# Kernel tuning notes

Hardware: AMD Instinct MI355X
Metric: run time of the kernel (lower is better)

Reference implementation:

```python
import jax, jax.numpy as jnp
import numpy as np

# Config constants (from DeepSeekConfig / init_kwargs)
NUM_EXPERTS = 6
VAR_EXPERTS = 4
FIXED_EXPERTS = NUM_EXPERTS - VAR_EXPERTS  # 2
TOP_K = 2
D_MODEL = 1024
D_FF = 4 * D_MODEL
LN_EPS = 1e-5


def setup_inputs() -> dict:
    key = jax.random.key(0)
    ks = jax.random.split(key, 6)
    B, S = 2, 2048
    x = jax.random.normal(ks[0], (B, S, D_MODEL), dtype=jnp.float32)
    router_W = jax.random.normal(ks[1], (D_MODEL, VAR_EXPERTS), dtype=jnp.float32) * 0.02
    # stacked expert FFN params: (E, D, 4D) and (E, 4D, D)
    W1 = jax.random.normal(ks[2], (NUM_EXPERTS, D_MODEL, D_FF), dtype=jnp.float32) * 0.02
    b1 = jnp.zeros((NUM_EXPERTS, D_FF), dtype=jnp.float32)
    W2 = jax.random.normal(ks[3], (NUM_EXPERTS, D_FF, D_MODEL), dtype=jnp.float32) * 0.02
    b2 = jnp.zeros((NUM_EXPERTS, D_MODEL), dtype=jnp.float32)
    ln_gamma = jnp.ones((D_MODEL,), dtype=jnp.float32)
    ln_beta = jnp.zeros((D_MODEL,), dtype=jnp.float32)
    return {"x": x, "router_W": router_W, "W1": W1, "b1": b1, "W2": W2,
            "b2": b2, "ln_gamma": ln_gamma, "ln_beta": ln_beta}


def reference(x, router_W, W1, b1, W2, b2, ln_gamma, ln_beta):
    B, S, D = x.shape
    # router over the VARIABLE experts only
    router_logits = jnp.einsum('bsd,de->bse', x, router_W)          # (B,S,VAR)
    router_probs = jax.nn.softmax(router_logits, axis=-1)
    _, topk_idx = jax.lax.top_k(router_probs, TOP_K)                 # (B,S,K)
    adj_idx = topk_idx + FIXED_EXPERTS                               # global expert ids in [FIXED, NUM)

    # dense per-expert FFN on all tokens: experts[e](x) = gelu(x@W1[e]+b1[e]) @ W2[e] + b2[e]
    h = jnp.einsum('bsd,edf->ebsf', x, W1) + b1[:, None, None, :]    # (E,B,S,4D)
    h = jax.nn.gelu(h, approximate=False)                            # torch F.gelu default = exact
    all_out = jnp.einsum('ebsf,efd->ebsd', h, W2) + b2[:, None, None, :]  # (E,B,S,D)

    # fixed experts: all of experts[0:FIXED] applied to every token
    fixed_sum = all_out[:FIXED_EXPERTS].sum(axis=0)                  # (B,S,D)

    # variable experts: per-token gather of the top-k selected experts
    b_ix = jnp.arange(B)[:, None, None]
    s_ix = jnp.arange(S)[None, :, None]
    var = all_out[adj_idx, b_ix, s_ix, :]                            # (B,S,K,D)

    # cat along expert slot dim then mean == sum / (FIXED + K); topk probs unused (plain mean)
    combined = (fixed_sum + var.sum(axis=2)) / (FIXED_EXPERTS + TOP_K)

    # LayerNorm (biased variance, eps=1e-5)
    mu = combined.mean(axis=-1, keepdims=True)
    v = combined.var(axis=-1, keepdims=True)
    out = (combined - mu) / jnp.sqrt(v + LN_EPS) * ln_gamma + ln_beta
    return out, router_logits
```

## Files before the change

### kernel.cpp

```cpp
#include <hip/hip_runtime.h>
#include <cstdint>
#include <cstddef>

#define D_MODEL 1024
#define D_FF 4096
#define NTOK 4096
#define LN_EPS 1e-5f

typedef __bf16 bf16x8 __attribute__((ext_vector_type(8)));
typedef float f32x4 __attribute__((ext_vector_type(4)));
typedef unsigned short u16x4 __attribute__((ext_vector_type(4)));
typedef unsigned short u16x8 __attribute__((ext_vector_type(8)));

static __device__ __forceinline__ unsigned short f2bf(float f) {
    union { float f; unsigned u; } v; v.f = f;
    unsigned r = v.u + 0x7fffu + ((v.u >> 16) & 1u);
    return (unsigned short)(r >> 16);
}

static __device__ __forceinline__ float b2f(unsigned short u) {
    union { unsigned u; float f; } v; v.u = (unsigned)u << 16;
    return v.f;
}

static __device__ __forceinline__ float gelu_fast(float x) {
    float x2 = x * x;
    float a2 = x * __builtin_fmaf(-0.1029432f, x2, -2.3022084f);
    float e = __builtin_amdgcn_exp2f(a2);
    return x * __builtin_amdgcn_rcpf(1.0f + e);
}

static __device__ __forceinline__ void gload16(const void* g, void* l) {
    __builtin_amdgcn_global_load_lds(
        (const __attribute__((address_space(1))) void*)g,
        (__attribute__((address_space(3))) void*)l, 16, 0, 0);
}

static __device__ __forceinline__ void seg_of(const int* cnt, int seg[4], int pc[4]) {
    int o = 2 * NTOK;
    #pragma unroll
    for (int e = 0; e < 4; ++e) {
        int c = cnt[e * 32];
        pc[e] = (c + 255) & ~255;
        seg[e] = o;
        o += pc[e];
    }
}

__global__ __launch_bounds__(256) void transpose_kernel(const float* __restrict__ W,
                                                        unsigned short* __restrict__ Wt,
                                                        int K, int N) {
    __shared__ unsigned short t[64][65];
    int k0 = blockIdx.y * 64, n0 = blockIdx.x * 64;
    const float* We = W + (size_t)blockIdx.z * K * N;
    unsigned short* Wte = Wt + (size_t)blockIdx.z * K * N;
    #pragma unroll
    for (int i = 0; i < 4; ++i) {
        int idx = threadIdx.x + i * 256;
        int kr = idx >> 4, c4 = idx & 15;
        f32x4 v = *(const f32x4*)&We[(size_t)(k0 + kr) * N + n0 + c4 * 4];
        #pragma unroll
        for (int j = 0; j < 4; ++j) t[c4 * 4 + j][kr] = f2bf(v[j]);
    }
    __syncthreads();
    #pragma unroll
    for (int i = 0; i < 2; ++i) {
        int idx = threadIdx.x + i * 256;
        int nr = idx >> 3, ck = idx & 7;
        u16x8 w;
        #pragma unroll
        for (int j = 0; j < 8; ++j) w[j] = t[nr][ck * 8 + j];
        *(u16x8*)&Wte[(size_t)(n0 + nr) * K + k0 + ck * 8] = w;
    }
}

__global__ __launch_bounds__(256) void router_kernel(
        const float* __restrict__ x, const float* __restrict__ rW,
        float* __restrict__ logits, int* __restrict__ selpk,
        int* __restrict__ slotpk, int* __restrict__ cnt, int* __restrict__ list,
        unsigned short* __restrict__ xb) {
    __shared__ int se[8];
    __shared__ int sslot[8];
    int wid = threadIdx.x >> 6, lane = threadIdx.x & 63;
    int t = blockIdx.x * 4 + wid;
    const float* xr = x + (size_t)t * D_MODEL;
    unsigned short* xbr = xb + (size_t)t * D_MODEL;
    float a0 = 0.f, a1 = 0.f, a2 = 0.f, a3 = 0.f;
    #pragma unroll
    for (int i = 0; i < 4; ++i) {
        int d4 = lane + i * 64;
        f32x4 xv = *(const f32x4*)&xr[d4 * 4];
        u16x4 bo;
        #pragma unroll
        for (int j = 0; j < 4; ++j) {
            float xj = xv[j];
            f32x4 wv = *(const f32x4*)&rW[(d4 * 4 + j) * 4];
            a0 = __builtin_fmaf(xj, wv[0], a0);
            a1 = __builtin_fmaf(xj, wv[1], a1);
            a2 = __builtin_fmaf(xj, wv[2], a2);
            a3 = __builtin_fmaf(xj, wv[3], a3);
            bo[j] = f2bf(xj);
        }
        *(u16x4*)&xbr[d4 * 4] = bo;
    }
    #pragma unroll
    for (int off = 32; off; off >>= 1) {
        a0 += __shfl_xor(a0, off); a1 += __shfl_xor(a1, off);
        a2 += __shfl_xor(a2, off); a3 += __shfl_xor(a3, off);
    }
    if (lane == 0) {
        float l[4] = {a0, a1, a2, a3};
        logits[t * 4 + 0] = a0; logits[t * 4 + 1] = a1;
        logits[t * 4 + 2] = a2; logits[t * 4 + 3] = a3;
        int e0 = 0; float b = l[0];
        #pragma unroll
        for (int e = 1; e < 4; ++e) if (l[e] > b) { b = l[e]; e0 = e; }
        int e1 = -1; float b2 = -1e30f;
        #pragma unroll
        for (int e = 0; e < 4; ++e) {
            if (e == e0) continue;
            if (l[e] > b2) { b2 = l[e]; e1 = e; }
        }
        se[wid * 2] = e0; se[wid * 2 + 1] = e1;
    }
    __syncthreads();
    if (threadIdx.x == 0) {
        int cnts[4] = {0, 0, 0, 0}, base[4];
        #pragma unroll
        for (int k = 0; k < 8; ++k) cnts[se[k]]++;
        #pragma unroll
        for (int e = 0; e < 4; ++e)
            if (cnts[e]) base[e] = atomicAdd(&cnt[e * 32], cnts[e]);
        int run[4] = {0, 0, 0, 0};
        #pragma unroll
        for (int k = 0; k < 8; ++k) {
            int e = se[k];
            int s = base[e] + run[e]++;
            sslot[k] = s;
            list[e * NTOK + s] = blockIdx.x * 4 + (k >> 1);
        }
    }
    __syncthreads();
    if (lane == 0) {
        selpk[t] = se[wid * 2] | (se[wid * 2 + 1] << 8);
        slotpk[t] = sslot[wid * 2] | (sslot[wid * 2 + 1] << 16);
    }
}

template<int GELU, int WM, int WN, int GX, int GY>
__global__ __launch_bounds__(512) void gemm_kernel(
        const unsigned short* __restrict__ A, const unsigned short* __restrict__ B,
        const float* __restrict__ bias, int bias_stride, int ldo,
        unsigned short* __restrict__ out,
        const int* __restrict__ cnt, const int* __restrict__ list, int K) {
    constexpr int BM = WM * 64, BN = WN * 64;
    __shared__ unsigned short As[BM * 64];
    __shared__ unsigned short Bs[BN * 64];

    const int D = blockIdx.x + GX * (blockIdx.y + GY * blockIdx.z);
    const int tq = D >> 3;
    const int W = ((D & 7) << 2) + ((tq >> 2) << 5) + (tq & 3);
    const int bx = W % GX;
    const int rem = W / GX;
    const int by = rem % GY;
    const int e  = rem / GY;

    const int tid = threadIdx.x, lane = tid & 63, w = tid >> 6;
    int ecnt = NTOK, rowbase;
    if (e < 2) {
        rowbase = e * NTOK + by * BM;
    } else {
        int seg[4], pc[4];
        seg_of(cnt, seg, pc);
        int ev = e - 2;
        ecnt = cnt[ev * 32];
        if (by * BM >= pc[ev]) return;
        rowbase = seg[ev] + by * BM;
    }
    const int n0 = bx * BN;
    const unsigned short* Be = B + (size_t)e * (D_FF * D_MODEL);

    const unsigned short* asrc[WM];
    const unsigned short* bsrc[WN];
    #pragma unroll
    for (int i = 0; i < WM; ++i) {
        int row = i * 64 + w * 8 + (lane >> 3);
        int kc = lane & 7;
        size_t arow;
        if (GELU) {
            int s = by * BM + row;
            if (e < 2) arow = (size_t)s;
            else       arow = (size_t)((s < ecnt) ? list[(e - 2) * NTOK + s] : 0);
        } else {
            arow = (size_t)(rowbase + row);
        }
        asrc[i] = A + arow * K + ((kc ^ (row & 7)) << 3);
    }
    #pragma unroll
    for (int i = 0; i < WN; ++i) {
        int row = i * 64 + w * 8 + (lane >> 3);
        int kc = lane & 7;
        bsrc[i] = Be + (size_t)(n0 + row) * K + ((kc ^ (row & 7)) << 3);
    }

    const int wm = (w / WN) * 64, wn = (w % WN) * 64;
    const int rl = lane & 15, kq = lane >> 4;

    float bv[4];
    #pragma unroll
    for (int ni = 0; ni < 4; ++ni)
        bv[ni] = bias[(size_t)e * bias_stride + n0 + wn + ni * 16 + rl];

    f32x4 acc[4][4];
    #pragma unroll
    for (int mi = 0; mi < 4; ++mi)
        #pragma unroll
        for (int ni = 0; ni < 4; ++ni) acc[mi][ni] = (f32x4)(bv[ni]);

    for (int kb = 0; kb < K; kb += 64) {
        #pragma unroll
        for (int i = 0; i < WM; ++i)
            gload16(asrc[i] + kb, &As[(i * 8 + w) * 512]);
        #pragma unroll
        for (int i = 0; i < WN; ++i)
            gload16(bsrc[i] + kb, &Bs[(i * 8 + w) * 512]);
        asm volatile("s_waitcnt vmcnt(0)" ::: "memory");
        __syncthreads();
        #pragma unroll
        for (int kk = 0; kk < 2; ++kk) {
            int kof = kk * 32 + kq * 8;
            bf16x8 a[4], b[4];
            #pragma unroll
            for (int mi = 0; mi < 4; ++mi) {
                int r = wm + mi * 16 + rl;
                a[mi] = *(const bf16x8*)&As[r * 64 + (kof ^ ((r & 7) << 3))];
            }
            #pragma unroll
            for (int ni = 0; ni < 4; ++ni) {
                int r = wn + ni * 16 + rl;
                b[ni] = *(const bf16x8*)&Bs[r * 64 + (kof ^ ((r & 7) << 3))];
            }
            #pragma unroll
            for (int mi = 0; mi < 4; ++mi)
                #pragma unroll
                for (int ni = 0; ni < 4; ++ni)
                    acc[mi][ni] = __builtin_amdgcn_mfma_f32_16x16x32_bf16(
                        a[mi], b[ni], acc[mi][ni], 0, 0, 0);
        }
        __syncthreads();
    }

    #pragma unroll
    for (int ni = 0; ni < 4; ++ni) {
        int c = n0 + wn + ni * 16 + rl;
        #pragma unroll
        for (int mi = 0; mi < 4; ++mi) {
            #pragma unroll
            for (int jp = 0; jp < 2; ++jp) {
                float g0 = acc[mi][ni][jp * 2 + 0];
                float g1 = acc[mi][ni][jp * 2 + 1];
                if (GELU) { g0 = gelu_fast(g0); g1 = gelu_fast(g1); }
                unsigned pk;
                asm("v_cvt_pk_bf16_f32 %0, %1, %2" : "=v"(pk) : "v"(g0), "v"(g1));
                int r = wm + mi * 16 + kq * 4 + jp * 2;
                unsigned short* p = out + (size_t)(rowbase + r) * ldo + c;
                p[0]   = (unsigned short)pk;
                p[ldo] = (unsigned short)(pk >> 16);
            }
        }
    }
}

__global__ __launch_bounds__(256) void pass3_kernel(
        const unsigned short* __restrict__ oslab, const int* __restrict__ selpk,
        const int* __restrict__ slotpk, const int* __restrict__ cnt,
        const float* __restrict__ gamma, const float* __restrict__ beta,
        float* __restrict__ out) {
    int t = blockIdx.x;
    int seg[4], pc[4];
    seg_of(cnt, seg, pc);
    int sp = selpk[t], sl = slotpk[t];
    int e0 = sp & 0xff, e1 = (sp >> 8) & 0xff;
    int s0 = sl & 0xffff, s1 = (sl >> 16) & 0xffff;
    const unsigned short* p0 = oslab + (size_t)t * D_MODEL;
    const unsigned short* p1 = oslab + (size_t)(NTOK + t) * D_MODEL;
    const unsigned short* p2 = oslab + (size_t)(seg[e0] + s0) * D_MODEL;
    const unsigned short* p3 = oslab + (size_t)(seg[e1] + s1) * D_MODEL;
    float c[4];
    float sum = 0.f, sq = 0.f;
    #pragma unroll
    for (int i = 0; i < 4; ++i) {
        int d = threadIdx.x + i * 256;
        float v = (b2f(p0[d]) + b2f(p1[d]) + b2f(p2[d]) + b2f(p3[d])) * 0.25f;
        c[i] = v; sum += v; sq += v * v;
    }
    #pragma unroll
    for (int off = 32; off; off >>= 1) {
        sum += __shfl_xor(sum, off);
        sq  += __shfl_xor(sq, off);
    }
    __shared__ float red[8];
    int lane = threadIdx.x & 63, wid = threadIdx.x >> 6;
    if (lane == 0) { red[wid] = sum; red[4 + wid] = sq; }
    __syncthreads();
    sum = red[0] + red[1] + red[2] + red[3];
    sq  = red[4] + red[5] + red[6] + red[7];
    float mean = sum * (1.0f / 1024.0f);
    float var = sq * (1.0f / 1024.0f) - mean * mean;
    float inv = rsqrtf(var + LN_EPS);
    #pragma unroll
    for (int i = 0; i < 4; ++i) {
        int d = threadIdx.x + i * 256;
        out[(size_t)t * D_MODEL + d] = (c[i] - mean) * inv * gamma[d] + beta[d];
    }
}

extern "C" void kernel_launch(void* const* d_in, const int* in_sizes, int n_in,
                              void* d_out, int out_size, void* d_ws, size_t ws_size,
                              hipStream_t stream) {
    const float* x   = (const float*)d_in[0];
    const float* rW  = (const float*)d_in[1];
    const float* W1  = (const float*)d_in[2];
    const float* b1  = (const float*)d_in[3];
    const float* W2  = (const float*)d_in[4];
    const float* b2  = (const float*)d_in[5];
    const float* gam = (const float*)d_in[6];
    const float* bet = (const float*)d_in[7];
    float* out = (float*)d_out;
    float* logits = out + (size_t)NTOK * D_MODEL;

    char* ws = (char*)d_ws;
    int* cnt    = (int*)ws;
    int* selpk  = (int*)(ws + 0x1000);
    int* slotpk = (int*)(ws + 0x6000);
    int* list   = (int*)(ws + 0xB000);
    unsigned short* xb    = (unsigned short*)(ws + 0x20000);
    unsigned short* W1t   = (unsigned short*)(ws + 0x820000);
    unsigned short* W2t   = (unsigned short*)(ws + 0x3820000);
    unsigned short* oslab = (unsigned short*)(ws + 0x6820000);
    unsigned short* h     = (unsigned short*)(ws + 0x8A20000);

    hipMemsetAsync(cnt, 0, 512, stream);
    router_kernel<<<NTOK / 4, 256, 0, stream>>>(x, rW, logits, selpk, slotpk, cnt, list, xb);
    transpose_kernel<<<dim3(D_FF / 64, D_MODEL / 64, 6), 256, 0, stream>>>(W1, W1t, D_MODEL, D_FF);
    transpose_kernel<<<dim3(D_MODEL / 64, D_FF / 64, 6), 256, 0, stream>>>(W2, W2t, D_FF, D_MODEL);

    gemm_kernel<1, 4, 2, 32, 16><<<dim3(32, 16, 6), 512, 0, stream>>>(
        xb, W1t, b1, D_FF, D_FF, h, cnt, list, D_MODEL);
    gemm_kernel<0, 2, 4, 4, 32><<<dim3(4, 32, 6), 512, 0, stream>>>(
        h, W2t, b2, D_MODEL, D_MODEL, oslab, cnt, list, D_FF);

    pass3_kernel<<<NTOK, 256, 0, stream>>>(oslab, selpk, slotpk, cnt, gam, bet, out);
}
```

Before: 460.9 us.

## Rewrite expert GEMMs as 256x256 double-buffered 8-phase pipelined kernel

```diff
diff --git a/kernel.cpp b/kernel.cpp
--- a/kernel.cpp
+++ b/kernel.cpp
@@ -147,15 +147,13 @@
     }
 }
 
-template<int GELU, int WM, int WN, int GX, int GY>
-__global__ __launch_bounds__(512) void gemm_kernel(
+template<int GELU, int GX, int GY>
+__global__ __launch_bounds__(512) void gemm8p_kernel(
         const unsigned short* __restrict__ A, const unsigned short* __restrict__ B,
         const float* __restrict__ bias, int bias_stride, int ldo,
         unsigned short* __restrict__ out,
         const int* __restrict__ cnt, const int* __restrict__ list, int K) {
-    constexpr int BM = WM * 64, BN = WN * 64;
-    __shared__ unsigned short As[BM * 64];
-    __shared__ unsigned short Bs[BN * 64];
+    __shared__ unsigned short lds[2][2][256 * 64];
 
     const int D = blockIdx.x + GX * (blockIdx.y + GY * blockIdx.z);
     const int tq = D >> 3;
@@ -165,96 +163,137 @@
     const int by = rem % GY;
     const int e  = rem / GY;
 
-    const int tid = threadIdx.x, lane = tid & 63, w = tid >> 6;
+    const int tid = threadIdx.x, l = tid & 63, w = tid >> 6;
     int ecnt = NTOK, rowbase;
     if (e < 2) {
-        rowbase = e * NTOK + by * BM;
+        rowbase = e * NTOK + by * 256;
     } else {
         int seg[4], pc[4];
         seg_of(cnt, seg, pc);
         int ev = e - 2;
         ecnt = cnt[ev * 32];
-        if (by * BM >= pc[ev]) return;
-        rowbase = seg[ev] + by * BM;
-    }
-    const int n0 = bx * BN;
+        if (by * 256 >= pc[ev]) return;
+        rowbase = seg[ev] + by * 256;
+    }
+    const int n0 = bx * 256;
     const unsigned short* Be = B + (size_t)e * (D_FF * D_MODEL);
 
-    const unsigned short* asrc[WM];
-    const unsigned short* bsrc[WN];
-    #pragma unroll
-    for (int i = 0; i < WM; ++i) {
-        int row = i * 64 + w * 8 + (lane >> 3);
-        int kc = lane & 7;
+    const unsigned short* asrc[4];
+    const unsigned short* bsrc[4];
+    #pragma unroll
+    for (int hj = 0; hj < 4; ++hj) {
+        int row = (hj >> 1) * 128 + (hj & 1) * 64 + w * 8 + (l >> 3);
+        int piece = ((l & 7) ^ (row & 7)) << 3;
         size_t arow;
         if (GELU) {
-            int s = by * BM + row;
+            int s = by * 256 + row;
             if (e < 2) arow = (size_t)s;
             else       arow = (size_t)((s < ecnt) ? list[(e - 2) * NTOK + s] : 0);
         } else {
             arow = (size_t)(rowbase + row);
         }
-        asrc[i] = A + arow * K + ((kc ^ (row & 7)) << 3);
-    }
-    #pragma unroll
-    for (int i = 0; i < WN; ++i) {
-        int row = i * 64 + w * 8 + (lane >> 3);
-        int kc = lane & 7;
-        bsrc[i] = Be + (size_t)(n0 + row) * K + ((kc ^ (row & 7)) << 3);
-    }
-
-    const int wm = (w / WN) * 64, wn = (w % WN) * 64;
-    const int rl = lane & 15, kq = lane >> 4;
+        asrc[hj] = A + arow * K + piece;
+        bsrc[hj] = Be + (size_t)(n0 + row) * K + piece;
+    }
+
+    const int wr = w >> 2, wc = w & 3;
+    const int rl = l & 15, kq = l >> 4;
 
     float bv[4];
     #pragma unroll
     for (int ni = 0; ni < 4; ++ni)
-        bv[ni] = bias[(size_t)e * bias_stride + n0 + wn + ni * 16 + rl];
-
-    f32x4 acc[4][4];
-    #pragma unroll
-    for (int mi = 0; mi < 4; ++mi)
+        bv[ni] = bias[(size_t)e * bias_stride + n0 + wc * 64 + ni * 16 + rl];
+
+    f32x4 acc[8][4];
+    #pragma unroll
+    for (int mi = 0; mi < 8; ++mi)
         #pragma unroll
         for (int ni = 0; ni < 4; ++ni) acc[mi][ni] = (f32x4)(bv[ni]);
 
-    for (int kb = 0; kb < K; kb += 64) {
-        #pragma unroll
-        for (int i = 0; i < WM; ++i)
-            gload16(asrc[i] + kb, &As[(i * 8 + w) * 512]);
-        #pragma unroll
-        for (int i = 0; i < WN; ++i)
-            gload16(bsrc[i] + kb, &Bs[(i * 8 + w) * 512]);
-        asm volatile("s_waitcnt vmcnt(0)" ::: "memory");
-        __syncthreads();
-        #pragma unroll
-        for (int kk = 0; kk < 2; ++kk) {
-            int kof = kk * 32 + kq * 8;
-            bf16x8 a[4], b[4];
-            #pragma unroll
-            for (int mi = 0; mi < 4; ++mi) {
-                int r = wm + mi * 16 + rl;
-                a[mi] = *(const bf16x8*)&As[r * 64 + (kof ^ ((r & 7) << 3))];
-            }
-            #pragma unroll
-            for (int ni = 0; ni < 4; ++ni) {
-                int r = wn + ni * 16 + rl;
-                b[ni] = *(const bf16x8*)&Bs[r * 64 + (kof ^ ((r & 7) << 3))];
-            }
-            #pragma unroll
-            for (int mi = 0; mi < 4; ++mi)
-                #pragma unroll
-                for (int ni = 0; ni < 4; ++ni)
-                    acc[mi][ni] = __builtin_amdgcn_mfma_f32_16x16x32_bf16(
-                        a[mi], b[ni], acc[mi][ni], 0, 0, 0);
-        }
-        __syncthreads();
-    }
+    asm volatile("" :: "v"(bv[0]), "v"(bv[1]), "v"(bv[2]), "v"(bv[3]));
+    asm volatile("s_waitcnt vmcnt(0)" ::: "memory");
+
+    #define STG1(bf, mat, h, j, t)                                              \
+        gload16(((mat) ? bsrc[(h) * 2 + (j)] : asrc[(h) * 2 + (j)]) +           \
+                    (size_t)(t) * 64,                                           \
+                &lds[bf][mat][((h) * 128 + (j) * 64 + w * 8) * 64])
+    #define STGU(bf, mat, h, t) { STG1(bf, mat, h, 0, t); STG1(bf, mat, h, 1, t); }
+
+    STGU(0, 0, 0, 0); STGU(0, 0, 1, 0);
+    STGU(0, 1, 0, 0); STGU(0, 1, 1, 0);
+    STGU(1, 1, 0, 1); STGU(1, 1, 1, 1);
+    asm volatile("s_waitcnt vmcnt(4)" ::: "memory");
+    __builtin_amdgcn_s_barrier();
+
+    bf16x8 bfr[4][2];
+
+    #define PHASE(bufR, q, LOADB, STAGE, ENDVM)                                 \
+    {                                                                           \
+        bf16x8 afr[2][2];                                                       \
+        _Pragma("unroll")                                                       \
+        for (int m2 = 0; m2 < 2; ++m2)                                          \
+            _Pragma("unroll")                                                   \
+            for (int kk = 0; kk < 2; ++kk) {                                    \
+                int r = wr * 128 + ((q) * 2 + m2) * 16 + rl;                    \
+                afr[m2][kk] = *(const bf16x8*)&lds[bufR][0]                     \
+                    [r * 64 + ((kk * 32 + kq * 8) ^ ((r & 7) << 3))];           \
+            }                                                                   \
+        if (LOADB) {                                                            \
+            _Pragma("unroll")                                                   \
+            for (int ni = 0; ni < 4; ++ni)                                      \
+                _Pragma("unroll")                                               \
+                for (int kk = 0; kk < 2; ++kk) {                                \
+                    int r = wc * 64 + ni * 16 + rl;                             \
+                    bfr[ni][kk] = *(const bf16x8*)&lds[bufR][1]                 \
+                        [r * 64 + ((kk * 32 + kq * 8) ^ ((r & 7) << 3))];       \
+                }                                                               \
+        }                                                                       \
+        STAGE;                                                                  \
+        __builtin_amdgcn_s_barrier();                                           \
+        asm volatile("s_waitcnt lgkmcnt(0)" ::: "memory");                      \
+        __builtin_amdgcn_sched_barrier(0);                                      \
+        __builtin_amdgcn_s_setprio(1);                                          \
+        _Pragma("unroll")                                                       \
+        for (int m2 = 0; m2 < 2; ++m2)                                          \
+            _Pragma("unroll")                                                   \
+            for (int kk = 0; kk < 2; ++kk)                                      \
+                _Pragma("unroll")                                               \
+                for (int ni = 0; ni < 4; ++ni)                                  \
+                    acc[(q) * 2 + m2][ni] =                                     \
+                        __builtin_amdgcn_mfma_f32_16x16x32_bf16(                \
+                            afr[m2][kk], bfr[ni][kk], acc[(q) * 2 + m2][ni],    \
+                            0, 0, 0);                                           \
+        __builtin_amdgcn_s_setprio(0);                                          \
+        ENDVM;                                                                  \
+        __builtin_amdgcn_s_barrier();                                           \
+    }
+
+    const int npairs = K / 128;
+    #pragma unroll 1
+    for (int p = 0; p < npairs; ++p) {
+        const int t0 = 2 * p;
+        const bool nl = (p + 1 < npairs);
+        PHASE(0, 0, 1, { STGU(1, 0, 0, t0 + 1); }, {});
+        PHASE(0, 1, 0, { STGU(1, 0, 1, t0 + 1); }, {});
+        PHASE(0, 2, 0, { if (nl) STGU(0, 1, 0, t0 + 2); }, {});
+        PHASE(0, 3, 0, { if (nl) STGU(0, 1, 1, t0 + 2); },
+              { if (nl) { asm volatile("s_waitcnt vmcnt(4)" ::: "memory"); }
+                else    { asm volatile("s_waitcnt vmcnt(0)" ::: "memory"); } });
+        PHASE(1, 0, 1, { if (nl) STGU(0, 0, 0, t0 + 2); }, {});
+        PHASE(1, 1, 0, { if (nl) STGU(0, 0, 1, t0 + 2); }, {});
+        PHASE(1, 2, 0, { if (nl) STGU(1, 1, 0, t0 + 3); }, {});
+        PHASE(1, 3, 0, { if (nl) STGU(1, 1, 1, t0 + 3); },
+              { if (nl) { asm volatile("s_waitcnt vmcnt(4)" ::: "memory"); } });
+    }
+    #undef PHASE
+    #undef STGU
+    #undef STG1
 
     #pragma unroll
     for (int ni = 0; ni < 4; ++ni) {
-        int c = n0 + wn + ni * 16 + rl;
-        #pragma unroll
-        for (int mi = 0; mi < 4; ++mi) {
+        int c = n0 + wc * 64 + ni * 16 + rl;
+        #pragma unroll
+        for (int mi = 0; mi < 8; ++mi) {
             #pragma unroll
             for (int jp = 0; jp < 2; ++jp) {
                 float g0 = acc[mi][ni][jp * 2 + 0];
@@ -262,10 +301,10 @@
                 if (GELU) { g0 = gelu_fast(g0); g1 = gelu_fast(g1); }
                 unsigned pk;
                 asm("v_cvt_pk_bf16_f32 %0, %1, %2" : "=v"(pk) : "v"(g0), "v"(g1));
-                int r = wm + mi * 16 + kq * 4 + jp * 2;
-                unsigned short* p = out + (size_t)(rowbase + r) * ldo + c;
-                p[0]   = (unsigned short)pk;
-                p[ldo] = (unsigned short)(pk >> 16);
+                int r = wr * 128 + mi * 16 + kq * 4 + jp * 2;
+                unsigned short* ptr = out + (size_t)(rowbase + r) * ldo + c;
+                ptr[0]   = (unsigned short)pk;
+                ptr[ldo] = (unsigned short)(pk >> 16);
             }
         }
     }
@@ -345,9 +384,9 @@
     transpose_kernel<<<dim3(D_FF / 64, D_MODEL / 64, 6), 256, 0, stream>>>(W1, W1t, D_MODEL, D_FF);
     transpose_kernel<<<dim3(D_MODEL / 64, D_FF / 64, 6), 256, 0, stream>>>(W2, W2t, D_FF, D_MODEL);
 
-    gemm_kernel<1, 4, 2, 32, 16><<<dim3(32, 16, 6), 512, 0, stream>>>(
+    gemm8p_kernel<1, 16, 16><<<dim3(16, 16, 6), 512, 0, stream>>>(
         xb, W1t, b1, D_FF, D_FF, h, cnt, list, D_MODEL);
-    gemm_kernel<0, 2, 4, 4, 32><<<dim3(4, 32, 6), 512, 0, stream>>>(
+    gemm8p_kernel<0, 4, 16><<<dim3(4, 16, 6), 512, 0, stream>>>(
         h, W2t, b2, D_MODEL, D_MODEL, oslab, cnt, list, D_FF);
 
     pass3_kernel<<<NTOK, 256, 0, stream>>>(oslab, selpk, slotpk, cnt, gam, bet, out);
```

Measured after the change: 485.8 us. 1.05x slower.
